# Performance work log

Hardware: AMD Instinct MI355X
Metric: run time of the kernel (lower is better)

Reference implementation:

```python
import jax, jax.numpy as jnp
import numpy as np

B, S, OUT = 256, 256, 64
IN = 4 * S * S


def setup_inputs() -> dict:
    key = jax.random.key(0)
    k1, k2, k3 = jax.random.split(key, 3)
    x = jax.random.normal(k1, (B, IN), dtype=jnp.float32)
    # nn.Linear init scale ~ 1/sqrt(fan_in); exact distribution irrelevant for correctness
    W = jax.random.normal(k2, (OUT, IN), dtype=jnp.float32) * (1.0 / np.sqrt(IN))
    b = jax.random.normal(k3, (OUT,), dtype=jnp.float32) * (1.0 / np.sqrt(IN))
    return {"x": x, "W": W, "b": b}


def _haar_dwt2_features(x):
    # x: [B, 4*S*S] viewed as [B, 4, S, S]; single-level Haar dwt2 per channel.
    # pywt haar: approx=(e+o)/sqrt2, detail=(e-o)/sqrt2 along each axis =>
    # with 2x2 block [[a,b],[c,d]]: LL=(a+b+c+d)/2, cH=(a+b-c-d)/2,
    # cV=(a-b+c-d)/2, cD=(a-b-c+d)/2; code concatenates [LL, cH, cV, cD]
    # per channel, then channels.
    Bn = x.shape[0]
    s = int(np.sqrt(x.shape[1] // 4))
    x4 = x.reshape(Bn, 4, s, s)
    a = x4[:, :, 0::2, 0::2]
    bq = x4[:, :, 0::2, 1::2]
    c = x4[:, :, 1::2, 0::2]
    d = x4[:, :, 1::2, 1::2]
    LL = (a + bq + c + d) * 0.5
    LH = (a + bq - c - d) * 0.5  # pywt cH
    HL = (a - bq + c - d) * 0.5  # pywt cV
    HH = (a - bq - c + d) * 0.5  # pywt cD
    # [B, 4ch, 4subband, s/2, s/2] -> flatten: channel-major, subband next
    t = jnp.stack([LL, LH, HL, HH], axis=2)
    return t.reshape(Bn, -1)


def reference(x, W, b):
    t = _haar_dwt2_features(x)
    # original wraps transform in torch.no_grad()
    t = jax.lax.stop_gradient(t)
    return t @ W.T + b
```

## Files before the change

kernel.cpp:

```cpp
#include <hip/hip_runtime.h>
#include <hip/hip_bf16.h>
#include <stdint.h>


#define IN_K  262144
#define PITCH 264

typedef short bf16x8 __attribute__((ext_vector_type(8)));
typedef float f32x4  __attribute__((ext_vector_type(4)));

__device__ __forceinline__ uint32_t pack2_bf16(float a, float b) {
    uint32_t ua = __float_as_uint(a);
    uint32_t ub = __float_as_uint(b);
    ua = (ua + 0x7fffu + ((ua >> 16) & 1u)) >> 16;
    ub = (ub + 0x7fffu + ((ub >> 16) & 1u)) >> 16;
    return ua | (ub << 16);
}

__global__ __launch_bounds__(512, 4) void wavelet_gemm(
    const float* __restrict__ x, const float* __restrict__ W,
    float* __restrict__ part)
{
    __shared__ short Ash[64 * PITCH];
    __shared__ short Bsh[64 * PITCH];

    const int tid  = threadIdx.x;
    const int lane = tid & 63;
    const int l16  = lane & 15;
    const int l4   = lane >> 4;
    const int wave = tid >> 6;

    const int b  = blockIdx.x;
    const int mh = b & 3;
    const int s  = b >> 2;
    const int jh = s & 1;
    const int i  = (s >> 1) & 127;
    const int c  = s >> 8;

    const float* xbase = x + (size_t)mh * 64 * IN_K
                           + c * 65536 + 2 * i * 256 + 128 * jh;
#pragma unroll
    for (int r = 0; r < 4; r++) {
        const int p   = tid + 512 * r;
        const int m_l = p >> 5;
        const int jj4 = p & 31;
        const float* xp = xbase + (size_t)m_l * IN_K + 4 * jj4;
        const float4 f0 = *(const float4*)(xp);
        const float4 f1 = *(const float4*)(xp + 256);
        const float s1 = f0.x + f0.y, d1 = f0.x - f0.y;
        const float s2 = f1.x + f1.y, d2 = f1.x - f1.y;
        const float t1 = f0.z + f0.w, e1 = f0.z - f0.w;
        const float t2 = f1.z + f1.w, e2 = f1.z - f1.w;
        union { bf16x8 v; uint32_t u[4]; } au;
        au.u[0] = pack2_bf16(s1 + s2, s1 - s2);
        au.u[1] = pack2_bf16(d1 + d2, d1 - d2);
        au.u[2] = pack2_bf16(t1 + t2, t1 - t2);
        au.u[3] = pack2_bf16(e1 + e2, e1 - e2);
        *(bf16x8*)&Ash[m_l * PITCH + 8 * jj4] = au.v;
    }

    const float* wbase = W + c * 65536 + i * 128 + 64 * jh;
#pragma unroll
    for (int r = 0; r < 2; r++) {
        const int slot = tid + 512 * r;
        const int n    = slot >> 4;
        const int jlq  = slot & 15;
        const float* wp = wbase + (size_t)n * IN_K + 4 * jlq;
        const float4 v0 = *(const float4*)(wp);
        const float4 v1 = *(const float4*)(wp + 16384);
        const float4 v2 = *(const float4*)(wp + 32768);
        const float4 v3 = *(const float4*)(wp + 49152);
        union { bf16x8 v; uint32_t u[4]; } b0, b1;
        b0.u[0] = pack2_bf16(v0.x, v1.x);
        b0.u[1] = pack2_bf16(v2.x, v3.x);
        b0.u[2] = pack2_bf16(v0.y, v1.y);
        b0.u[3] = pack2_bf16(v2.y, v3.y);
        b1.u[0] = pack2_bf16(v0.z, v1.z);
        b1.u[1] = pack2_bf16(v2.z, v3.z);
        b1.u[2] = pack2_bf16(v0.w, v1.w);
        b1.u[3] = pack2_bf16(v2.w, v3.w);
        *(bf16x8*)&Bsh[n * PITCH + 16 * jlq]     = b0.v;
        *(bf16x8*)&Bsh[n * PITCH + 16 * jlq + 8] = b1.v;
    }

    __syncthreads();

    const int tm = wave & 3;
    const int nh = wave >> 2;
    f32x4 acc0 = (f32x4){0.f, 0.f, 0.f, 0.f};
    f32x4 acc1 = (f32x4){0.f, 0.f, 0.f, 0.f};
#pragma unroll
    for (int kh = 0; kh < 8; kh++) {
        const int ko = kh * 32 + l4 * 8;
        bf16x8 a  = *(const bf16x8*)&Ash[(tm * 16 + l16) * PITCH + ko];
        bf16x8 b0 = *(const bf16x8*)&Bsh[(nh * 32 + l16) * PITCH + ko];
        bf16x8 b1 = *(const bf16x8*)&Bsh[(nh * 32 + 16 + l16) * PITCH + ko];
        acc0 = __builtin_amdgcn_mfma_f32_16x16x32_bf16(a, b0, acc0, 0, 0, 0);
        acc1 = __builtin_amdgcn_mfma_f32_16x16x32_bf16(a, b1, acc1, 0, 0, 0);
    }

    float* pp = part + (size_t)b * 4096;
#pragma unroll
    for (int r = 0; r < 4; r++) {
        const int m = tm * 16 + l4 * 4 + r;
        pp[m * 64 + nh * 32 + l16]      = acc0[r];
        pp[m * 64 + nh * 32 + 16 + l16] = acc1[r];
    }
}

__global__ __launch_bounds__(512) void wavelet_reduce(
    const float* __restrict__ part, const float* __restrict__ bias,
    float* __restrict__ out)
{
    __shared__ float red[8][64];
    const int m  = blockIdx.x;
    const int mh = m >> 6;
    const int ml = m & 63;
    const int n  = threadIdx.x & 63;
    const int g  = threadIdx.x >> 6;
    const float* base = part + (size_t)ml * 64 + n + (size_t)mh * 4096;
    float acc = 0.f;
#pragma unroll 4
    for (int s = g; s < 1024; s += 8)
        acc += base[(size_t)s * 4 * 4096];
    red[g][n] = acc;
    __syncthreads();
    if (g == 0) {
        float v = red[0][n] + red[1][n] + red[2][n] + red[3][n]
                + red[4][n] + red[5][n] + red[6][n] + red[7][n];
        out[m * 64 + n] = 0.5f * v + bias[n];
    }
}

extern "C" void kernel_launch(void* const* d_in, const int* in_sizes, int n_in,
                              void* d_out, int out_size, void* d_ws, size_t ws_size,
                              hipStream_t stream)
{
    const float* x = (const float*)d_in[0];
    const float* W = (const float*)d_in[1];
    const float* b = (const float*)d_in[2];
    float* out  = (float*)d_out;
    float* part = (float*)d_ws;

    wavelet_gemm<<<4096, 512, 0, stream>>>(x, W, part);
    wavelet_reduce<<<256, 512, 0, stream>>>(part, b, out);
}
```

Before: 441.9 us.

## Loop eight K-chunks per GEMM block with register prefetch, shrink split-K partials

Each GEMM block now handles eight consecutive K-chunks instead of one, cutting the grid from 4096 to 512 blocks. Global loads for the next chunk are issued into registers before the MFMA loop over the current chunk, so memory latency can overlap compute. This also shrinks the partial-sum buffer by a factor of eight and makes the reduce kernel lighter. The costs are more registers for the prefetch buffers, two barriers per chunk, and only 512 blocks, which may leave the GPU's compute units underfilled.

Result: faster. 428.8 us (-3.0%).

```diff
diff --git a/kernel.cpp b/kernel.cpp
--- a/kernel.cpp
+++ b/kernel.cpp
@@ -30,73 +30,99 @@
     const int l4   = lane >> 4;
     const int wave = tid >> 6;
 
-    const int b  = blockIdx.x;
-    const int mh = b & 3;
-    const int s  = b >> 2;
-    const int jh = s & 1;
-    const int i  = (s >> 1) & 127;
-    const int c  = s >> 8;
+    const int b    = blockIdx.x;
+    const int mh   = b & 3;
+    const int widx = b >> 2;
+    const int c    = widx >> 5;
+    const int ig   = widx & 31;
 
-    const float* xbase = x + (size_t)mh * 64 * IN_K
-                           + c * 65536 + 2 * i * 256 + 128 * jh;
+    const float* xm  = x + (size_t)(mh * 64) * IN_K + c * 65536;
+    const float* wcb = W + c * 65536;
+
+    const int a_m  = tid >> 5;
+    const int a_j4 = tid & 31;
+    const int b_n  = tid >> 4;
+    const int b_j  = tid & 15;
+
+    float4 af[4][2];
+    float4 bf[2][4];
+
+    auto load_chunk = [&](int t) {
+        const int i  = ig * 4 + (t >> 1);
+        const int jh = t & 1;
+        const float* xc = xm + 2 * i * 256 + 128 * jh;
 #pragma unroll
-    for (int r = 0; r < 4; r++) {
-        const int p   = tid + 512 * r;
-        const int m_l = p >> 5;
-        const int jj4 = p & 31;
-        const float* xp = xbase + (size_t)m_l * IN_K + 4 * jj4;
-        const float4 f0 = *(const float4*)(xp);
-        const float4 f1 = *(const float4*)(xp + 256);
-        const float s1 = f0.x + f0.y, d1 = f0.x - f0.y;
-        const float s2 = f1.x + f1.y, d2 = f1.x - f1.y;
-        const float t1 = f0.z + f0.w, e1 = f0.z - f0.w;
-        const float t2 = f1.z + f1.w, e2 = f1.z - f1.w;
-        union { bf16x8 v; uint32_t u[4]; } au;
-        au.u[0] = pack2_bf16(s1 + s2, s1 - s2);
-        au.u[1] = pack2_bf16(d1 + d2, d1 - d2);
-        au.u[2] = pack2_bf16(t1 + t2, t1 - t2);
-        au.u[3] = pack2_bf16(e1 + e2, e1 - e2);
-        *(bf16x8*)&Ash[m_l * PITCH + 8 * jj4] = au.v;
-    }
+        for (int r = 0; r < 4; r++) {
+            const float* xp = xc + (size_t)(a_m + 16 * r) * IN_K + 4 * a_j4;
+            af[r][0] = *(const float4*)(xp);
+            af[r][1] = *(const float4*)(xp + 256);
+        }
+        const float* wc = wcb + i * 128 + 64 * jh;
+#pragma unroll
+        for (int r = 0; r < 2; r++) {
+            const float* wp = wc + (size_t)(b_n + 32 * r) * IN_K + 4 * b_j;
+            bf[r][0] = *(const float4*)(wp);
+            bf[r][1] = *(const float4*)(wp + 16384);
+            bf[r][2] = *(const float4*)(wp + 32768);
+            bf[r][3] = *(const float4*)(wp + 49152);
+        }
+    };
 
-    const float* wbase = W + c * 65536 + i * 128 + 64 * jh;
+    auto stage = [&]() {
 #pragma unroll
-    for (int r = 0; r < 2; r++) {
-        const int slot = tid + 512 * r;
-        const int n    = slot >> 4;
-        const int jlq  = slot & 15;
-        const float* wp = wbase + (size_t)n * IN_K + 4 * jlq;
-        const float4 v0 = *(const float4*)(wp);
-        const float4 v1 = *(const float4*)(wp + 16384);
-        const float4 v2 = *(const float4*)(wp + 32768);
-        const float4 v3 = *(const float4*)(wp + 49152);
-        union { bf16x8 v; uint32_t u[4]; } b0, b1;
-        b0.u[0] = pack2_bf16(v0.x, v1.x);
-        b0.u[1] = pack2_bf16(v2.x, v3.x);
-        b0.u[2] = pack2_bf16(v0.y, v1.y);
-        b0.u[3] = pack2_bf16(v2.y, v3.y);
-        b1.u[0] = pack2_bf16(v0.z, v1.z);
-        b1.u[1] = pack2_bf16(v2.z, v3.z);
-        b1.u[2] = pack2_bf16(v0.w, v1.w);
-        b1.u[3] = pack2_bf16(v2.w, v3.w);
-        *(bf16x8*)&Bsh[n * PITCH + 16 * jlq]     = b0.v;
-        *(bf16x8*)&Bsh[n * PITCH + 16 * jlq + 8] = b1.v;
-    }
-
-    __syncthreads();
+        for (int r = 0; r < 4; r++) {
+            const float4 f0 = af[r][0], f1 = af[r][1];
+            const float s1 = f0.x + f0.y, d1 = f0.x - f0.y;
+            const float s2 = f1.x + f1.y, d2 = f1.x - f1.y;
+            const float t1 = f0.z + f0.w, e1 = f0.z - f0.w;
+            const float t2 = f1.z + f1.w, e2 = f1.z - f1.w;
+            union { bf16x8 v; uint32_t u[4]; } au;
+            au.u[0] = pack2_bf16(s1 + s2, s1 - s2);
+            au.u[1] = pack2_bf16(d1 + d2, d1 - d2);
+            au.u[2] = pack2_bf16(t1 + t2, t1 - t2);
+            au.u[3] = pack2_bf16(e1 + e2, e1 - e2);
+            *(bf16x8*)&Ash[(a_m + 16 * r) * PITCH + 8 * a_j4] = au.v;
+        }
+#pragma unroll
+        for (int r = 0; r < 2; r++) {
+            const float4 v0 = bf[r][0], v1 = bf[r][1];
+            const float4 v2 = bf[r][2], v3 = bf[r][3];
+            union { bf16x8 v; uint32_t u[4]; } b0, b1;
+            b0.u[0] = pack2_bf16(v0.x, v1.x);
+            b0.u[1] = pack2_bf16(v2.x, v3.x);
+            b0.u[2] = pack2_bf16(v0.y, v1.y);
+            b0.u[3] = pack2_bf16(v2.y, v3.y);
+            b1.u[0] = pack2_bf16(v0.z, v1.z);
+            b1.u[1] = pack2_bf16(v2.z, v3.z);
+            b1.u[2] = pack2_bf16(v0.w, v1.w);
+            b1.u[3] = pack2_bf16(v2.w, v3.w);
+            short* br = &Bsh[(b_n + 32 * r) * PITCH + 16 * b_j];
+            *(bf16x8*)(br)     = b0.v;
+            *(bf16x8*)(br + 8) = b1.v;
+        }
+    };
 
     const int tm = wave & 3;
     const int nh = wave >> 2;
     f32x4 acc0 = (f32x4){0.f, 0.f, 0.f, 0.f};
     f32x4 acc1 = (f32x4){0.f, 0.f, 0.f, 0.f};
+
+    load_chunk(0);
+#pragma unroll 1
+    for (int t = 0; t < 8; t++) {
+        stage();
+        __syncthreads();
+        if (t < 7) load_chunk(t + 1);
 #pragma unroll
-    for (int kh = 0; kh < 8; kh++) {
-        const int ko = kh * 32 + l4 * 8;
-        bf16x8 a  = *(const bf16x8*)&Ash[(tm * 16 + l16) * PITCH + ko];
-        bf16x8 b0 = *(const bf16x8*)&Bsh[(nh * 32 + l16) * PITCH + ko];
-        bf16x8 b1 = *(const bf16x8*)&Bsh[(nh * 32 + 16 + l16) * PITCH + ko];
-        acc0 = __builtin_amdgcn_mfma_f32_16x16x32_bf16(a, b0, acc0, 0, 0, 0);
-        acc1 = __builtin_amdgcn_mfma_f32_16x16x32_bf16(a, b1, acc1, 0, 0, 0);
+        for (int kh = 0; kh < 8; kh++) {
+            const int ko = kh * 32 + l4 * 8;
+            bf16x8 a  = *(const bf16x8*)&Ash[(tm * 16 + l16) * PITCH + ko];
+            bf16x8 bb0 = *(const bf16x8*)&Bsh[(nh * 32 + l16) * PITCH + ko];
+            bf16x8 bb1 = *(const bf16x8*)&Bsh[(nh * 32 + 16 + l16) * PITCH + ko];
+            acc0 = __builtin_amdgcn_mfma_f32_16x16x32_bf16(a, bb0, acc0, 0, 0, 0);
+            acc1 = __builtin_amdgcn_mfma_f32_16x16x32_bf16(a, bb1, acc1, 0, 0, 0);
+        }
+        __syncthreads();
     }
 
     float* pp = part + (size_t)b * 4096;
@@ -108,26 +134,25 @@
     }
 }
 
-__global__ __launch_bounds__(512) void wavelet_reduce(
+__global__ __launch_bounds__(256) void wavelet_reduce(
     const float* __restrict__ part, const float* __restrict__ bias,
     float* __restrict__ out)
 {
-    __shared__ float red[8][64];
+    __shared__ float red[4][64];
     const int m  = blockIdx.x;
     const int mh = m >> 6;
     const int ml = m & 63;
     const int n  = threadIdx.x & 63;
     const int g  = threadIdx.x >> 6;
-    const float* base = part + (size_t)ml * 64 + n + (size_t)mh * 4096;
+    const float* base = part + (size_t)mh * 4096 + ml * 64 + n;
     float acc = 0.f;
 #pragma unroll 4
-    for (int s = g; s < 1024; s += 8)
-        acc += base[(size_t)s * 4 * 4096];
+    for (int w = g; w < 128; w += 4)
+        acc += base[(size_t)w * 16384];
     red[g][n] = acc;
     __syncthreads();
     if (g == 0) {
-        float v = red[0][n] + red[1][n] + red[2][n] + red[3][n]
-                + red[4][n] + red[5][n] + red[6][n] + red[7][n];
+        const float v = red[0][n] + red[1][n] + red[2][n] + red[3][n];
         out[m * 64 + n] = 0.5f * v + bias[n];
     }
 }
@@ -142,6 +167,6 @@
     float* out  = (float*)d_out;
     float* part = (float*)d_ws;
 
-    wavelet_gemm<<<4096, 512, 0, stream>>>(x, W, part);
-    wavelet_reduce<<<256, 512, 0, stream>>>(part, b, out);
+    wavelet_gemm<<<512, 512, 0, stream>>>(x, W, part);
+    wavelet_reduce<<<256, 256, 0, stream>>>(part, b, out);
 }
```
